# Kernel optimization log

Measured on AMD Instinct MI355X. Metric: run time of the kernel, lower is better.

The kernel has to match this reference:

```python
import jax, jax.numpy as jnp
import numpy as np

# SMPL-style skeleton: parent index per joint (parent < child, root = -1)
PARENTS = [-1, 0, 0, 0, 1, 2, 3, 4, 5, 6, 7, 8, 9, 9, 9, 12, 13, 14, 16, 17, 18, 19, 20, 21]
END_SITES = [10, 11, 15, 22, 23]  # feet, head, hands
NUM_JOINTS = len(PARENTS)


def rot6d_to_matrix(x):
    """6D rotation rep -> 3x3 matrix via Gram-Schmidt. x: [..., 6] -> [..., 3, 3].
    eye(3).reshape(-1)[:6] = [1,0,0,0,1,0] maps to identity under this (row-stacked) convention."""
    a1, a2 = x[..., 0:3], x[..., 3:6]
    b1 = a1 / jnp.linalg.norm(a1, axis=-1, keepdims=True)
    a2p = a2 - jnp.sum(b1 * a2, axis=-1, keepdims=True) * b1
    b2 = a2p / jnp.linalg.norm(a2p, axis=-1, keepdims=True)
    b3 = jnp.cross(b1, b2)
    return jnp.stack([b1, b2, b3], axis=-2)


def fk_positions(rot, offsets):
    """Forward kinematics (faithful to _recompute_joint_global_info).
    rot: [F, J, 3, 3] local joint rotations; offsets: [F, J, 3].
    Returns global joint positions [F, J, 3]. Loop is over the fixed, small
    joint hierarchy (structural), fully vectorized over frames."""
    positions = [offsets[:, 0]]          # root: offset only
    orientations = [rot[:, 0]]           # root: local rotation
    for i in range(1, NUM_JOINTS):
        pi = PARENTS[i]
        po = orientations[pi]            # [F, 3, 3]
        pos = jnp.einsum('fab,fb->fa', po, offsets[:, i]) + positions[pi]
        positions.append(pos)
        orientations.append(po @ rot[:, i])
    return jnp.stack(positions, axis=1)  # [F, J, 3]


def setup_inputs() -> dict:
    key = jax.random.key(0)
    ks = jax.random.split(key, 6)
    F = 65536
    return {
        'poseA': jax.random.normal(ks[0], (F, NUM_JOINTS, 6), dtype=jnp.float32),
        'poseB': jax.random.normal(ks[1], (F, NUM_JOINTS, 6), dtype=jnp.float32),
        'joint_offsets_A': jax.random.normal(ks[2], (F, NUM_JOINTS, 3), dtype=jnp.float32),
        'joint_offsets_B': jax.random.normal(ks[3], (F, NUM_JOINTS, 3), dtype=jnp.float32),
        't_poseA': jax.random.normal(ks[4], (NUM_JOINTS, 3), dtype=jnp.float32),
        't_poseB': jax.random.normal(ks[5], (NUM_JOINTS, 3), dtype=jnp.float32),
    }


def reference(poseA, poseB, joint_offsets_A, joint_offsets_B, t_poseA, t_poseB):
    ee = jnp.array(END_SITES)
    # 6D -> rotation matrices (to_matrix)
    RA = rot6d_to_matrix(poseA)
    RB = rot6d_to_matrix(poseB)
    # sequential per-joint FK (the hot loop)
    posA = fk_positions(RA, joint_offsets_A)
    posB = fk_positions(RB, joint_offsets_B)
    # bbox scale from T-pose
    scale_A = jnp.max(t_poseA, axis=0) - jnp.min(t_poseA, axis=0)  # [3]
    scale_B = jnp.max(t_poseB, axis=0) - jnp.min(t_poseB, axis=0)
    eeA = posA[:, ee, :] - t_poseA[ee, :]   # [F, E, 3]
    eeB = posB[:, ee, :] - t_poseB[ee, :]
    loss = jnp.mean((eeA / scale_A - eeB / scale_B) ** 2)
    return loss
```

## Files before the change

kernel.cpp:

```cpp
#include <hip/hip_runtime.h>


struct V3 { float x, y, z; };
struct M3 { float m[3][3]; };

__device__ __forceinline__ V3 matvec(const M3& A, const V3& v) {
    return { A.m[0][0]*v.x + A.m[0][1]*v.y + A.m[0][2]*v.z,
             A.m[1][0]*v.x + A.m[1][1]*v.y + A.m[1][2]*v.z,
             A.m[2][0]*v.x + A.m[2][1]*v.y + A.m[2][2]*v.z };
}

__device__ __forceinline__ M3 matmul(const M3& A, const M3& B) {
    M3 C;
#pragma unroll
    for (int i = 0; i < 3; i++)
#pragma unroll
        for (int j = 0; j < 3; j++)
            C.m[i][j] = A.m[i][0]*B.m[0][j] + A.m[i][1]*B.m[1][j] + A.m[i][2]*B.m[2][j];
    return C;
}

#define PROW 25
#define OROW 13

struct FK { M3 o; V3 p; };

__device__ __forceinline__ M3 rot6d_lds(const float* __restrict__ rp, int base) {
    float v0 = rp[base+0], v1 = rp[base+1], v2 = rp[base+2];
    float v3 = rp[base+3], v4 = rp[base+4], v5 = rp[base+5];
    float n1 = v0*v0 + v1*v1 + v2*v2;
    float r1 = 1.0f / sqrtf(n1);
    V3 b1 = { v0*r1, v1*r1, v2*r1 };
    float d = b1.x*v3 + b1.y*v4 + b1.z*v5;
    V3 u = { v3 - d*b1.x, v4 - d*b1.y, v5 - d*b1.z };
    float n2 = u.x*u.x + u.y*u.y + u.z*u.z;
    float r2 = 1.0f / sqrtf(n2);
    V3 b2 = { u.x*r2, u.y*r2, u.z*r2 };
    V3 b3 = { b1.y*b2.z - b1.z*b2.y, b1.z*b2.x - b1.x*b2.z, b1.x*b2.y - b1.y*b2.x };
    M3 R;
    R.m[0][0]=b1.x; R.m[0][1]=b1.y; R.m[0][2]=b1.z;
    R.m[1][0]=b2.x; R.m[1][1]=b2.y; R.m[1][2]=b2.z;
    R.m[2][0]=b3.x; R.m[2][1]=b3.y; R.m[2][2]=b3.z;
    return R;
}

__device__ __forceinline__ FK fk_step_l(const float* __restrict__ rp,
                                        const float* __restrict__ ro,
                                        int pb, int ob, const FK& par) {
    V3 off = { ro[ob], ro[ob+1], ro[ob+2] };
    V3 t = matvec(par.o, off);
    FK s;
    s.p = { par.p.x + t.x, par.p.y + t.y, par.p.z + t.z };
    s.o = matmul(par.o, rot6d_lds(rp, pb));
    return s;
}

__device__ __forceinline__ V3 fk_end_l(const float* __restrict__ ro,
                                       int ob, const FK& par) {
    V3 off = { ro[ob], ro[ob+1], ro[ob+2] };
    V3 t = matvec(par.o, off);
    return { par.p.x + t.x, par.p.y + t.y, par.p.z + t.z };
}

__global__ __launch_bounds__(256)
void ee_loss_kernel(const float* __restrict__ poseA, const float* __restrict__ poseB,
                    const float* __restrict__ offA,  const float* __restrict__ offB,
                    const float* __restrict__ tA,    const float* __restrict__ tB,
                    float* __restrict__ out, float inv_count) {
    __shared__ float s_pose[4][64 * PROW];
    __shared__ float s_off [4][64 * OROW];
    __shared__ float s_eeB[128][15];
    __shared__ float s_inv[6];
    __shared__ float s_d[15];
    __shared__ float s_part[2];

    const int tid  = threadIdx.x;
    const int wid  = tid >> 6;
    const int lane = tid & 63;
    const bool isB = wid & 1;
    const int fg   = wid >> 1;
    const int fl   = fg * 64 + lane;
    const long long f0 = (long long)blockIdx.x * 128 + fg * 64;

    const float* __restrict__ P = (isB ? poseB : poseA) + f0 * 144;
    const float* __restrict__ O = (isB ? offB  : offA ) + f0 * 72;

    float* sp = s_pose[wid];
    float* so = s_off[wid];
    const float* rp = sp + lane * PROW;
    const float* ro = so + lane * OROW;

    if (tid < 6) {
        const float* tp = (tid < 3) ? tA : tB;
        int ax = (tid < 3) ? tid : tid - 3;
        float mn = tp[ax], mx = mn;
#pragma unroll
        for (int j = 1; j < 24; j++) {
            float v = tp[j*3 + ax];
            mn = fminf(mn, v); mx = fmaxf(mx, v);
        }
        s_inv[tid] = 1.0f / (mx - mn);
    }
    if (tid < 15) {
        const int EE[5] = {10, 11, 15, 22, 23};
        int e = tid / 3, ax = tid - 3*e;
        int j = EE[e];
        float mnA = tA[ax], mxA = mnA, mnB = tB[ax], mxB = mnB;
#pragma unroll
        for (int k = 1; k < 24; k++) {
            float a = tA[k*3 + ax], b = tB[k*3 + ax];
            mnA = fminf(mnA, a); mxA = fmaxf(mxA, a);
            mnB = fminf(mnB, b); mxB = fmaxf(mxB, b);
        }
        s_d[tid] = tB[j*3 + ax]/(mxB - mnB) - tA[j*3 + ax]/(mxA - mnA);
    }

    auto stageP = [&](int st) {
#pragma unroll
        for (int k = 0; k < 6; k++) {
            int idx = lane + 64 * k;
            int f = idx / 6, c = idx - 6 * f;
            float4 v = *(const float4*)(P + f*144 + st*24 + c*4);
            float* d = sp + f*PROW + c*4;
            d[0] = v.x; d[1] = v.y; d[2] = v.z; d[3] = v.w;
        }
#pragma unroll
        for (int k = 0; k < 6; k++) {
            int idx = lane + 64 * k;
            int f = idx / 6, c = idx - 6 * f;
            float2 v = *(const float2*)(O + f*72 + st*12 + c*2);
            float* d = so + f*OROW + c*2;
            d[0] = v.x; d[1] = v.y;
        }
    };

    stageP(0);
    FK s0; s0.o = rot6d_lds(rp, 0); s0.p = { ro[0], ro[1], ro[2] };
    FK s1 = fk_step_l(rp, ro,  6, 3, s0);
    FK s2 = fk_step_l(rp, ro, 12, 6, s0);
    FK s3 = fk_step_l(rp, ro, 18, 9, s0);

    stageP(1);
    FK s4 = fk_step_l(rp, ro,  0, 0, s1);
    FK s5 = fk_step_l(rp, ro,  6, 3, s2);
    FK s6 = fk_step_l(rp, ro, 12, 6, s3);
    FK s7 = fk_step_l(rp, ro, 18, 9, s4);

    stageP(2);
    FK s8 = fk_step_l(rp, ro,  0, 0, s5);
    FK s9 = fk_step_l(rp, ro,  6, 3, s6);
    V3 e10 = fk_end_l(ro, 6, s7);
    V3 e11 = fk_end_l(ro, 9, s8);

    stageP(3);
    FK s12 = fk_step_l(rp, ro,  0, 0, s9);
    FK s13 = fk_step_l(rp, ro,  6, 3, s9);
    FK s14 = fk_step_l(rp, ro, 12, 6, s9);
    V3 e15 = fk_end_l(ro, 9, s12);

    stageP(4);
    FK s16 = fk_step_l(rp, ro,  0, 0, s13);
    FK s17 = fk_step_l(rp, ro,  6, 3, s14);
    FK s18 = fk_step_l(rp, ro, 12, 6, s16);
    FK s19 = fk_step_l(rp, ro, 18, 9, s17);

    stageP(5);
    FK s20 = fk_step_l(rp, ro,  0, 0, s18);
    FK s21 = fk_step_l(rp, ro,  6, 3, s19);
    V3 e22 = fk_end_l(ro, 6, s20);
    V3 e23 = fk_end_l(ro, 9, s21);

    if (isB) {
        s_eeB[fl][ 0] = e10.x; s_eeB[fl][ 1] = e10.y; s_eeB[fl][ 2] = e10.z;
        s_eeB[fl][ 3] = e11.x; s_eeB[fl][ 4] = e11.y; s_eeB[fl][ 5] = e11.z;
        s_eeB[fl][ 6] = e15.x; s_eeB[fl][ 7] = e15.y; s_eeB[fl][ 8] = e15.z;
        s_eeB[fl][ 9] = e22.x; s_eeB[fl][10] = e22.y; s_eeB[fl][11] = e22.z;
        s_eeB[fl][12] = e23.x; s_eeB[fl][13] = e23.y; s_eeB[fl][14] = e23.z;
    }
    __syncthreads();

    float local = 0.0f;
    if (!isB) {
        const float iax = s_inv[0], iay = s_inv[1], iaz = s_inv[2];
        const float ibx = s_inv[3], iby = s_inv[4], ibz = s_inv[5];
        const float* eb = s_eeB[fl];
        float t0  = e10.x*iax - eb[ 0]*ibx + s_d[ 0];
        float t1  = e10.y*iay - eb[ 1]*iby + s_d[ 1];
        float t2  = e10.z*iaz - eb[ 2]*ibz + s_d[ 2];
        float t3  = e11.x*iax - eb[ 3]*ibx + s_d[ 3];
        float t4  = e11.y*iay - eb[ 4]*iby + s_d[ 4];
        float t5  = e11.z*iaz - eb[ 5]*ibz + s_d[ 5];
        float t6  = e15.x*iax - eb[ 6]*ibx + s_d[ 6];
        float t7  = e15.y*iay - eb[ 7]*iby + s_d[ 7];
        float t8  = e15.z*iaz - eb[ 8]*ibz + s_d[ 8];
        float t9  = e22.x*iax - eb[ 9]*ibx + s_d[ 9];
        float t10 = e22.y*iay - eb[10]*iby + s_d[10];
        float t11 = e22.z*iaz - eb[11]*ibz + s_d[11];
        float t12 = e23.x*iax - eb[12]*ibx + s_d[12];
        float t13 = e23.y*iay - eb[13]*iby + s_d[13];
        float t14 = e23.z*iaz - eb[14]*ibz + s_d[14];
        local = ((t0*t0 + t1*t1) + (t2*t2 + t3*t3) + (t4*t4 + t5*t5) +
                 (t6*t6 + t7*t7) + (t8*t8 + t9*t9) + (t10*t10 + t11*t11) +
                 (t12*t12 + t13*t13) + t14*t14) * inv_count;
#pragma unroll
        for (int off = 32; off > 0; off >>= 1)
            local += __shfl_down(local, off, 64);
        if (lane == 0) s_part[fg] = local;
    }
    __syncthreads();
    if (tid == 0) atomicAdd(out, s_part[0] + s_part[1]);
}

extern "C" void kernel_launch(void* const* d_in, const int* in_sizes, int n_in,
                              void* d_out, int out_size, void* d_ws, size_t ws_size,
                              hipStream_t stream) {
    const float* poseA = (const float*)d_in[0];
    const float* poseB = (const float*)d_in[1];
    const float* offA  = (const float*)d_in[2];
    const float* offB  = (const float*)d_in[3];
    const float* tA    = (const float*)d_in[4];
    const float* tB    = (const float*)d_in[5];
    float* out = (float*)d_out;

    const int F = in_sizes[0] / 144;
    const int blocks = F / 128;
    const float inv_count = 1.0f / ((float)F * 15.0f);

    hipMemsetAsync(out, 0, sizeof(float), stream);
    ee_loss_kernel<<<blocks, 256, 0, stream>>>(poseA, poseB, offA, offB, tA, tB,
                                               out, inv_count);
}
```

Baseline: 146.6 us.

## Double-buffer stage loads in registers and use float4 LDS layout

Global loads for each joint stage are now issued two stages ahead into register buffers and written to LDS after the current stage's compute. This overlaps memory latency with the FK math. The LDS staging also switches to float4 rows with padded strides and vector reads, and offset loads go from float2 to float4. In exchange, register pressure rises from holding two stage buffers, and launch bounds now request 2 blocks per CU.

```diff
diff --git a/kernel.cpp b/kernel.cpp
--- a/kernel.cpp
+++ b/kernel.cpp
@@ -3,6 +3,7 @@
 
 struct V3 { float x, y, z; };
 struct M3 { float m[3][3]; };
+struct FK { M3 o; V3 p; };
 
 __device__ __forceinline__ V3 matvec(const M3& A, const V3& v) {
     return { A.m[0][0]*v.x + A.m[0][1]*v.y + A.m[0][2]*v.z,
@@ -20,14 +21,8 @@
     return C;
 }
 
-#define PROW 25
-#define OROW 13
-
-struct FK { M3 o; V3 p; };
-
-__device__ __forceinline__ M3 rot6d_lds(const float* __restrict__ rp, int base) {
-    float v0 = rp[base+0], v1 = rp[base+1], v2 = rp[base+2];
-    float v3 = rp[base+3], v4 = rp[base+4], v5 = rp[base+5];
+__device__ __forceinline__ M3 rot6d(float v0, float v1, float v2,
+                                    float v3, float v4, float v5) {
     float n1 = v0*v0 + v1*v1 + v2*v2;
     float r1 = 1.0f / sqrtf(n1);
     V3 b1 = { v0*r1, v1*r1, v2*r1 };
@@ -44,31 +39,71 @@
     return R;
 }
 
-__device__ __forceinline__ FK fk_step_l(const float* __restrict__ rp,
-                                        const float* __restrict__ ro,
-                                        int pb, int ob, const FK& par) {
-    V3 off = { ro[ob], ro[ob+1], ro[ob+2] };
-    V3 t = matvec(par.o, off);
+__device__ __forceinline__ FK fk_step(float a0,float a1,float a2,float a3,float a4,float a5,
+                                      float ox,float oy,float oz, const FK& par) {
+    V3 t = matvec(par.o, {ox, oy, oz});
     FK s;
     s.p = { par.p.x + t.x, par.p.y + t.y, par.p.z + t.z };
-    s.o = matmul(par.o, rot6d_lds(rp, pb));
+    s.o = matmul(par.o, rot6d(a0, a1, a2, a3, a4, a5));
     return s;
 }
 
-__device__ __forceinline__ V3 fk_end_l(const float* __restrict__ ro,
-                                       int ob, const FK& par) {
-    V3 off = { ro[ob], ro[ob+1], ro[ob+2] };
-    V3 t = matvec(par.o, off);
+__device__ __forceinline__ V3 fk_end(float ox, float oy, float oz, const FK& par) {
+    V3 t = matvec(par.o, {ox, oy, oz});
     return { par.p.x + t.x, par.p.y + t.y, par.p.z + t.z };
 }
 
-__global__ __launch_bounds__(256)
+#define PSTR 7
+#define OSTR 5
+
+struct SBuf { float4 p[6]; float4 o[3]; };
+
+__device__ __forceinline__ void load_stage(SBuf& b, const float* __restrict__ P,
+                                           const float* __restrict__ O,
+                                           int lane, int st) {
+#pragma unroll
+    for (int k = 0; k < 6; k++) {
+        int idx = lane + 64*k, f = idx/6, c = idx - 6*f;
+        b.p[k] = *(const float4*)(P + f*144 + st*24 + c*4);
+    }
+#pragma unroll
+    for (int k = 0; k < 3; k++) {
+        int idx = lane + 64*k, f = idx/3, c = idx - 3*f;
+        b.o[k] = *(const float4*)(O + f*72 + st*12 + c*4);
+    }
+}
+
+__device__ __forceinline__ void write_stage(const SBuf& b, float4* sp, float4* so, int lane) {
+#pragma unroll
+    for (int k = 0; k < 6; k++) {
+        int idx = lane + 64*k, f = idx/6, c = idx - 6*f;
+        sp[f*PSTR + c] = b.p[k];
+    }
+#pragma unroll
+    for (int k = 0; k < 3; k++) {
+        int idx = lane + 64*k, f = idx/3, c = idx - 3*f;
+        so[f*OSTR + c] = b.o[k];
+    }
+}
+
+#define READQ  q0 = rp[0]; q1 = rp[1]; q2 = rp[2]; q3 = rp[3]; q4 = rp[4]; q5 = rp[5]; \
+               r0 = ro[0]; r1 = ro[1]; r2 = ro[2];
+#define J0ROT  q0.x,q0.y,q0.z,q0.w,q1.x,q1.y
+#define J1ROT  q1.z,q1.w,q2.x,q2.y,q2.z,q2.w
+#define J2ROT  q3.x,q3.y,q3.z,q3.w,q4.x,q4.y
+#define J3ROT  q4.z,q4.w,q5.x,q5.y,q5.z,q5.w
+#define J0OFF  r0.x,r0.y,r0.z
+#define J1OFF  r0.w,r1.x,r1.y
+#define J2OFF  r1.z,r1.w,r2.x
+#define J3OFF  r2.y,r2.z,r2.w
+
+__global__ __launch_bounds__(256, 2)
 void ee_loss_kernel(const float* __restrict__ poseA, const float* __restrict__ poseB,
                     const float* __restrict__ offA,  const float* __restrict__ offB,
                     const float* __restrict__ tA,    const float* __restrict__ tB,
                     float* __restrict__ out, float inv_count) {
-    __shared__ float s_pose[4][64 * PROW];
-    __shared__ float s_off [4][64 * OROW];
+    __shared__ float4 s_pose[4][64 * PSTR];
+    __shared__ float4 s_off [4][64 * OSTR];
     __shared__ float s_eeB[128][15];
     __shared__ float s_inv[6];
     __shared__ float s_d[15];
@@ -85,10 +120,14 @@
     const float* __restrict__ P = (isB ? poseB : poseA) + f0 * 144;
     const float* __restrict__ O = (isB ? offB  : offA ) + f0 * 72;
 
-    float* sp = s_pose[wid];
-    float* so = s_off[wid];
-    const float* rp = sp + lane * PROW;
-    const float* ro = so + lane * OROW;
+    float4* sp = s_pose[wid];
+    float4* so = s_off[wid];
+    const float4* rp = sp + lane * PSTR;
+    const float4* ro = so + lane * OSTR;
+
+    SBuf bA, bB;
+    load_stage(bA, P, O, lane, 0);
+    load_stage(bB, P, O, lane, 1);
 
     if (tid < 6) {
         const float* tp = (tid < 3) ? tA : tB;
@@ -115,60 +154,54 @@
         s_d[tid] = tB[j*3 + ax]/(mxB - mnB) - tA[j*3 + ax]/(mxA - mnA);
     }
 
-    auto stageP = [&](int st) {
-#pragma unroll
-        for (int k = 0; k < 6; k++) {
-            int idx = lane + 64 * k;
-            int f = idx / 6, c = idx - 6 * f;
-            float4 v = *(const float4*)(P + f*144 + st*24 + c*4);
-            float* d = sp + f*PROW + c*4;
-            d[0] = v.x; d[1] = v.y; d[2] = v.z; d[3] = v.w;
-        }
-#pragma unroll
-        for (int k = 0; k < 6; k++) {
-            int idx = lane + 64 * k;
-            int f = idx / 6, c = idx - 6 * f;
-            float2 v = *(const float2*)(O + f*72 + st*12 + c*2);
-            float* d = so + f*OROW + c*2;
-            d[0] = v.x; d[1] = v.y;
-        }
-    };
-
-    stageP(0);
-    FK s0; s0.o = rot6d_lds(rp, 0); s0.p = { ro[0], ro[1], ro[2] };
-    FK s1 = fk_step_l(rp, ro,  6, 3, s0);
-    FK s2 = fk_step_l(rp, ro, 12, 6, s0);
-    FK s3 = fk_step_l(rp, ro, 18, 9, s0);
-
-    stageP(1);
-    FK s4 = fk_step_l(rp, ro,  0, 0, s1);
-    FK s5 = fk_step_l(rp, ro,  6, 3, s2);
-    FK s6 = fk_step_l(rp, ro, 12, 6, s3);
-    FK s7 = fk_step_l(rp, ro, 18, 9, s4);
-
-    stageP(2);
-    FK s8 = fk_step_l(rp, ro,  0, 0, s5);
-    FK s9 = fk_step_l(rp, ro,  6, 3, s6);
-    V3 e10 = fk_end_l(ro, 6, s7);
-    V3 e11 = fk_end_l(ro, 9, s8);
-
-    stageP(3);
-    FK s12 = fk_step_l(rp, ro,  0, 0, s9);
-    FK s13 = fk_step_l(rp, ro,  6, 3, s9);
-    FK s14 = fk_step_l(rp, ro, 12, 6, s9);
-    V3 e15 = fk_end_l(ro, 9, s12);
-
-    stageP(4);
-    FK s16 = fk_step_l(rp, ro,  0, 0, s13);
-    FK s17 = fk_step_l(rp, ro,  6, 3, s14);
-    FK s18 = fk_step_l(rp, ro, 12, 6, s16);
-    FK s19 = fk_step_l(rp, ro, 18, 9, s17);
-
-    stageP(5);
-    FK s20 = fk_step_l(rp, ro,  0, 0, s18);
-    FK s21 = fk_step_l(rp, ro,  6, 3, s19);
-    V3 e22 = fk_end_l(ro, 6, s20);
-    V3 e23 = fk_end_l(ro, 9, s21);
+    write_stage(bA, sp, so, lane);
+
+    float4 q0, q1, q2, q3, q4, q5, r0, r1, r2;
+
+    READQ;
+    load_stage(bA, P, O, lane, 2);
+    FK s0; s0.o = rot6d(J0ROT); s0.p = { r0.x, r0.y, r0.z };
+    FK s1 = fk_step(J1ROT, J1OFF, s0);
+    FK s2 = fk_step(J2ROT, J2OFF, s0);
+    FK s3 = fk_step(J3ROT, J3OFF, s0);
+    write_stage(bB, sp, so, lane);
+
+    READQ;
+    load_stage(bB, P, O, lane, 3);
+    FK s4 = fk_step(J0ROT, J0OFF, s1);
+    FK s5 = fk_step(J1ROT, J1OFF, s2);
+    FK s6 = fk_step(J2ROT, J2OFF, s3);
+    FK s7 = fk_step(J3ROT, J3OFF, s4);
+    write_stage(bA, sp, so, lane);
+
+    READQ;
+    load_stage(bA, P, O, lane, 4);
+    FK s8 = fk_step(J0ROT, J0OFF, s5);
+    FK s9 = fk_step(J1ROT, J1OFF, s6);
+    V3 e10 = fk_end(J2OFF, s7);
+    V3 e11 = fk_end(J3OFF, s8);
+    write_stage(bB, sp, so, lane);
+
+    READQ;
+    load_stage(bB, P, O, lane, 5);
+    FK s12 = fk_step(J0ROT, J0OFF, s9);
+    FK s13 = fk_step(J1ROT, J1OFF, s9);
+    FK s14 = fk_step(J2ROT, J2OFF, s9);
+    V3 e15 = fk_end(J3OFF, s12);
+    write_stage(bA, sp, so, lane);
+
+    READQ;
+    FK s16 = fk_step(J0ROT, J0OFF, s13);
+    FK s17 = fk_step(J1ROT, J1OFF, s14);
+    FK s18 = fk_step(J2ROT, J2OFF, s16);
+    FK s19 = fk_step(J3ROT, J3OFF, s17);
+    write_stage(bB, sp, so, lane);
+
+    READQ;
+    FK s20 = fk_step(J0ROT, J0OFF, s18);
+    FK s21 = fk_step(J1ROT, J1OFF, s19);
+    V3 e22 = fk_end(J2OFF, s20);
+    V3 e23 = fk_end(J3OFF, s21);
 
     if (isB) {
         s_eeB[fl][ 0] = e10.x; s_eeB[fl][ 1] = e10.y; s_eeB[fl][ 2] = e10.z;
```

Result: slower. 172.8 us (+17.9%).

## Load pose/offset data directly to registers and pair A/B frames via lane shuffles

Applied to the files above, without the earlier changes.

Drops the LDS staging of pose and offset data. Each thread now reads its own frame's rows straight from global memory into float4 registers, double-buffered across stages. A and B skeletons for the same frame are interleaved on adjacent lanes, so end-effector positions are exchanged with xor-shuffles instead of a shared-memory array. The per-block final reduction becomes one atomic per wavefront. Per-thread strided float4 loads lose the coalescing the staged path had, and register pressure rises, both of which may reduce memory efficiency.

```diff
diff --git a/kernel.cpp b/kernel.cpp
--- a/kernel.cpp
+++ b/kernel.cpp
@@ -3,6 +3,7 @@
 
 struct V3 { float x, y, z; };
 struct M3 { float m[3][3]; };
+struct FK { M3 o; V3 p; };
 
 __device__ __forceinline__ V3 matvec(const M3& A, const V3& v) {
     return { A.m[0][0]*v.x + A.m[0][1]*v.y + A.m[0][2]*v.z,
@@ -20,14 +21,8 @@
     return C;
 }
 
-#define PROW 25
-#define OROW 13
-
-struct FK { M3 o; V3 p; };
-
-__device__ __forceinline__ M3 rot6d_lds(const float* __restrict__ rp, int base) {
-    float v0 = rp[base+0], v1 = rp[base+1], v2 = rp[base+2];
-    float v3 = rp[base+3], v4 = rp[base+4], v5 = rp[base+5];
+__device__ __forceinline__ M3 rot6d(float v0, float v1, float v2,
+                                    float v3, float v4, float v5) {
     float n1 = v0*v0 + v1*v1 + v2*v2;
     float r1 = 1.0f / sqrtf(n1);
     V3 b1 = { v0*r1, v1*r1, v2*r1 };
@@ -44,51 +39,56 @@
     return R;
 }
 
-__device__ __forceinline__ FK fk_step_l(const float* __restrict__ rp,
-                                        const float* __restrict__ ro,
-                                        int pb, int ob, const FK& par) {
-    V3 off = { ro[ob], ro[ob+1], ro[ob+2] };
-    V3 t = matvec(par.o, off);
+__device__ __forceinline__ FK fk_step(float a0,float a1,float a2,float a3,float a4,float a5,
+                                      float ox,float oy,float oz, const FK& par) {
+    V3 t = matvec(par.o, {ox, oy, oz});
     FK s;
     s.p = { par.p.x + t.x, par.p.y + t.y, par.p.z + t.z };
-    s.o = matmul(par.o, rot6d_lds(rp, pb));
+    s.o = matmul(par.o, rot6d(a0, a1, a2, a3, a4, a5));
     return s;
 }
 
-__device__ __forceinline__ V3 fk_end_l(const float* __restrict__ ro,
-                                       int ob, const FK& par) {
-    V3 off = { ro[ob], ro[ob+1], ro[ob+2] };
-    V3 t = matvec(par.o, off);
+__device__ __forceinline__ V3 fk_end(float ox, float oy, float oz, const FK& par) {
+    V3 t = matvec(par.o, {ox, oy, oz});
     return { par.p.x + t.x, par.p.y + t.y, par.p.z + t.z };
 }
+
+#define LOADST(X, ST) do { \
+    X##q0 = *(const float4*)(P + (ST)*24 +  0); \
+    X##q1 = *(const float4*)(P + (ST)*24 +  4); \
+    X##q2 = *(const float4*)(P + (ST)*24 +  8); \
+    X##q3 = *(const float4*)(P + (ST)*24 + 12); \
+    X##q4 = *(const float4*)(P + (ST)*24 + 16); \
+    X##q5 = *(const float4*)(P + (ST)*24 + 20); \
+    X##r0 = *(const float4*)(O + (ST)*12 +  0); \
+    X##r1 = *(const float4*)(O + (ST)*12 +  4); \
+    X##r2 = *(const float4*)(O + (ST)*12 +  8); \
+} while (0)
+
+#define JR0(X) X##q0.x,X##q0.y,X##q0.z,X##q0.w,X##q1.x,X##q1.y
+#define JR1(X) X##q1.z,X##q1.w,X##q2.x,X##q2.y,X##q2.z,X##q2.w
+#define JR2(X) X##q3.x,X##q3.y,X##q3.z,X##q3.w,X##q4.x,X##q4.y
+#define JR3(X) X##q4.z,X##q4.w,X##q5.x,X##q5.y,X##q5.z,X##q5.w
+#define JO0(X) X##r0.x,X##r0.y,X##r0.z
+#define JO1(X) X##r0.w,X##r1.x,X##r1.y
+#define JO2(X) X##r1.z,X##r1.w,X##r2.x
+#define JO3(X) X##r2.y,X##r2.z,X##r2.w
 
 __global__ __launch_bounds__(256)
 void ee_loss_kernel(const float* __restrict__ poseA, const float* __restrict__ poseB,
                     const float* __restrict__ offA,  const float* __restrict__ offB,
                     const float* __restrict__ tA,    const float* __restrict__ tB,
                     float* __restrict__ out, float inv_count) {
-    __shared__ float s_pose[4][64 * PROW];
-    __shared__ float s_off [4][64 * OROW];
-    __shared__ float s_eeB[128][15];
     __shared__ float s_inv[6];
     __shared__ float s_d[15];
-    __shared__ float s_part[2];
 
     const int tid  = threadIdx.x;
-    const int wid  = tid >> 6;
-    const int lane = tid & 63;
-    const bool isB = wid & 1;
-    const int fg   = wid >> 1;
-    const int fl   = fg * 64 + lane;
-    const long long f0 = (long long)blockIdx.x * 128 + fg * 64;
-
-    const float* __restrict__ P = (isB ? poseB : poseA) + f0 * 144;
-    const float* __restrict__ O = (isB ? offB  : offA ) + f0 * 72;
-
-    float* sp = s_pose[wid];
-    float* so = s_off[wid];
-    const float* rp = sp + lane * PROW;
-    const float* ro = so + lane * OROW;
+    const long long t = (long long)blockIdx.x * 256 + tid;
+    const int  isB = (int)(t & 1);
+    const long long f = t >> 1;
+
+    const float* __restrict__ P = (isB ? poseB : poseA) + f * 144;
+    const float* __restrict__ O = (isB ? offB  : offA ) + f * 72;
 
     if (tid < 6) {
         const float* tp = (tid < 3) ? tA : tB;
@@ -115,100 +115,91 @@
         s_d[tid] = tB[j*3 + ax]/(mxB - mnB) - tA[j*3 + ax]/(mxA - mnA);
     }
 
-    auto stageP = [&](int st) {
-#pragma unroll
-        for (int k = 0; k < 6; k++) {
-            int idx = lane + 64 * k;
-            int f = idx / 6, c = idx - 6 * f;
-            float4 v = *(const float4*)(P + f*144 + st*24 + c*4);
-            float* d = sp + f*PROW + c*4;
-            d[0] = v.x; d[1] = v.y; d[2] = v.z; d[3] = v.w;
-        }
-#pragma unroll
-        for (int k = 0; k < 6; k++) {
-            int idx = lane + 64 * k;
-            int f = idx / 6, c = idx - 6 * f;
-            float2 v = *(const float2*)(O + f*72 + st*12 + c*2);
-            float* d = so + f*OROW + c*2;
-            d[0] = v.x; d[1] = v.y;
-        }
-    };
-
-    stageP(0);
-    FK s0; s0.o = rot6d_lds(rp, 0); s0.p = { ro[0], ro[1], ro[2] };
-    FK s1 = fk_step_l(rp, ro,  6, 3, s0);
-    FK s2 = fk_step_l(rp, ro, 12, 6, s0);
-    FK s3 = fk_step_l(rp, ro, 18, 9, s0);
-
-    stageP(1);
-    FK s4 = fk_step_l(rp, ro,  0, 0, s1);
-    FK s5 = fk_step_l(rp, ro,  6, 3, s2);
-    FK s6 = fk_step_l(rp, ro, 12, 6, s3);
-    FK s7 = fk_step_l(rp, ro, 18, 9, s4);
-
-    stageP(2);
-    FK s8 = fk_step_l(rp, ro,  0, 0, s5);
-    FK s9 = fk_step_l(rp, ro,  6, 3, s6);
-    V3 e10 = fk_end_l(ro, 6, s7);
-    V3 e11 = fk_end_l(ro, 9, s8);
-
-    stageP(3);
-    FK s12 = fk_step_l(rp, ro,  0, 0, s9);
-    FK s13 = fk_step_l(rp, ro,  6, 3, s9);
-    FK s14 = fk_step_l(rp, ro, 12, 6, s9);
-    V3 e15 = fk_end_l(ro, 9, s12);
-
-    stageP(4);
-    FK s16 = fk_step_l(rp, ro,  0, 0, s13);
-    FK s17 = fk_step_l(rp, ro,  6, 3, s14);
-    FK s18 = fk_step_l(rp, ro, 12, 6, s16);
-    FK s19 = fk_step_l(rp, ro, 18, 9, s17);
-
-    stageP(5);
-    FK s20 = fk_step_l(rp, ro,  0, 0, s18);
-    FK s21 = fk_step_l(rp, ro,  6, 3, s19);
-    V3 e22 = fk_end_l(ro, 6, s20);
-    V3 e23 = fk_end_l(ro, 9, s21);
-
-    if (isB) {
-        s_eeB[fl][ 0] = e10.x; s_eeB[fl][ 1] = e10.y; s_eeB[fl][ 2] = e10.z;
-        s_eeB[fl][ 3] = e11.x; s_eeB[fl][ 4] = e11.y; s_eeB[fl][ 5] = e11.z;
-        s_eeB[fl][ 6] = e15.x; s_eeB[fl][ 7] = e15.y; s_eeB[fl][ 8] = e15.z;
-        s_eeB[fl][ 9] = e22.x; s_eeB[fl][10] = e22.y; s_eeB[fl][11] = e22.z;
-        s_eeB[fl][12] = e23.x; s_eeB[fl][13] = e23.y; s_eeB[fl][14] = e23.z;
-    }
+    float4 aq0, aq1, aq2, aq3, aq4, aq5, ar0, ar1, ar2;
+    float4 bq0, bq1, bq2, bq3, bq4, bq5, br0, br1, br2;
+
+    LOADST(a, 0);
+    LOADST(b, 1);
+
+    FK s0; s0.o = rot6d(JR0(a)); s0.p = { ar0.x, ar0.y, ar0.z };
+    FK s1 = fk_step(JR1(a), JO1(a), s0);
+    FK s2 = fk_step(JR2(a), JO2(a), s0);
+    FK s3 = fk_step(JR3(a), JO3(a), s0);
+    LOADST(a, 2);
+
+    FK s4 = fk_step(JR0(b), JO0(b), s1);
+    FK s5 = fk_step(JR1(b), JO1(b), s2);
+    FK s6 = fk_step(JR2(b), JO2(b), s3);
+    FK s7 = fk_step(JR3(b), JO3(b), s4);
+    LOADST(b, 3);
+
+    FK s8 = fk_step(JR0(a), JO0(a), s5);
+    FK s9 = fk_step(JR1(a), JO1(a), s6);
+    V3 e10 = fk_end(JO2(a), s7);
+    V3 e11 = fk_end(JO3(a), s8);
+    LOADST(a, 4);
+
+    FK s12 = fk_step(JR0(b), JO0(b), s9);
+    FK s13 = fk_step(JR1(b), JO1(b), s9);
+    FK s14 = fk_step(JR2(b), JO2(b), s9);
+    V3 e15 = fk_end(JO3(b), s12);
+    LOADST(b, 5);
+
+    FK s16 = fk_step(JR0(a), JO0(a), s13);
+    FK s17 = fk_step(JR1(a), JO1(a), s14);
+    FK s18 = fk_step(JR2(a), JO2(a), s16);
+    FK s19 = fk_step(JR3(a), JO3(a), s17);
+
+    FK s20 = fk_step(JR0(b), JO0(b), s18);
+    FK s21 = fk_step(JR1(b), JO1(b), s19);
+    V3 e22 = fk_end(JO2(b), s20);
+    V3 e23 = fk_end(JO3(b), s21);
+
+    float p0  = __shfl_xor(e10.x, 1, 64);
+    float p1  = __shfl_xor(e10.y, 1, 64);
+    float p2  = __shfl_xor(e10.z, 1, 64);
+    float p3  = __shfl_xor(e11.x, 1, 64);
+    float p4  = __shfl_xor(e11.y, 1, 64);
+    float p5  = __shfl_xor(e11.z, 1, 64);
+    float p6  = __shfl_xor(e15.x, 1, 64);
+    float p7  = __shfl_xor(e15.y, 1, 64);
+    float p8  = __shfl_xor(e15.z, 1, 64);
+    float p9  = __shfl_xor(e22.x, 1, 64);
+    float p10 = __shfl_xor(e22.y, 1, 64);
+    float p11 = __shfl_xor(e22.z, 1, 64);
+    float p12 = __shfl_xor(e23.x, 1, 64);
+    float p13 = __shfl_xor(e23.y, 1, 64);
+    float p14 = __shfl_xor(e23.z, 1, 64);
+
     __syncthreads();
 
     float local = 0.0f;
     if (!isB) {
         const float iax = s_inv[0], iay = s_inv[1], iaz = s_inv[2];
         const float ibx = s_inv[3], iby = s_inv[4], ibz = s_inv[5];
-        const float* eb = s_eeB[fl];
-        float t0  = e10.x*iax - eb[ 0]*ibx + s_d[ 0];
-        float t1  = e10.y*iay - eb[ 1]*iby + s_d[ 1];
-        float t2  = e10.z*iaz - eb[ 2]*ibz + s_d[ 2];
-        float t3  = e11.x*iax - eb[ 3]*ibx + s_d[ 3];
-        float t4  = e11.y*iay - eb[ 4]*iby + s_d[ 4];
-        float t5  = e11.z*iaz - eb[ 5]*ibz + s_d[ 5];
-        float t6  = e15.x*iax - eb[ 6]*ibx + s_d[ 6];
-        float t7  = e15.y*iay - eb[ 7]*iby + s_d[ 7];
-        float t8  = e15.z*iaz - eb[ 8]*ibz + s_d[ 8];
-        float t9  = e22.x*iax - eb[ 9]*ibx + s_d[ 9];
-        float t10 = e22.y*iay - eb[10]*iby + s_d[10];
-        float t11 = e22.z*iaz - eb[11]*ibz + s_d[11];
-        float t12 = e23.x*iax - eb[12]*ibx + s_d[12];
-        float t13 = e23.y*iay - eb[13]*iby + s_d[13];
-        float t14 = e23.z*iaz - eb[14]*ibz + s_d[14];
+        float t0  = e10.x*iax - p0 *ibx + s_d[ 0];
+        float t1  = e10.y*iay - p1 *iby + s_d[ 1];
+        float t2  = e10.z*iaz - p2 *ibz + s_d[ 2];
+        float t3  = e11.x*iax - p3 *ibx + s_d[ 3];
+        float t4  = e11.y*iay - p4 *iby + s_d[ 4];
+        float t5  = e11.z*iaz - p5 *ibz + s_d[ 5];
+        float t6  = e15.x*iax - p6 *ibx + s_d[ 6];
+        float t7  = e15.y*iay - p7 *iby + s_d[ 7];
+        float t8  = e15.z*iaz - p8 *ibz + s_d[ 8];
+        float t9  = e22.x*iax - p9 *ibx + s_d[ 9];
+        float t10 = e22.y*iay - p10*iby + s_d[10];
+        float t11 = e22.z*iaz - p11*ibz + s_d[11];
+        float t12 = e23.x*iax - p12*ibx + s_d[12];
+        float t13 = e23.y*iay - p13*iby + s_d[13];
+        float t14 = e23.z*iaz - p14*ibz + s_d[14];
         local = ((t0*t0 + t1*t1) + (t2*t2 + t3*t3) + (t4*t4 + t5*t5) +
                  (t6*t6 + t7*t7) + (t8*t8 + t9*t9) + (t10*t10 + t11*t11) +
                  (t12*t12 + t13*t13) + t14*t14) * inv_count;
-#pragma unroll
-        for (int off = 32; off > 0; off >>= 1)
-            local += __shfl_down(local, off, 64);
-        if (lane == 0) s_part[fg] = local;
     }
-    __syncthreads();
-    if (tid == 0) atomicAdd(out, s_part[0] + s_part[1]);
+#pragma unroll
+    for (int off = 32; off > 0; off >>= 1)
+        local += __shfl_down(local, off, 64);
+    if ((tid & 63) == 0) atomicAdd(out, local);
 }
 
 extern "C" void kernel_launch(void* const* d_in, const int* in_sizes, int n_in,
@@ -223,7 +214,7 @@
     float* out = (float*)d_out;
 
     const int F = in_sizes[0] / 144;
-    const int blocks = F / 128;
+    const int blocks = (2 * F) / 256;
     const float inv_count = 1.0f / ((float)F * 15.0f);
 
     hipMemsetAsync(out, 0, sizeof(float), stream);
```

Result: slower. 174.3 us (+18.9%).
